# Kernel optimization log

Measured on AMD Instinct MI355X. Metric: run time of the kernel, lower is better.

Reference implementation:

```python
import jax, jax.numpy as jnp
import numpy as np

CLP_K = 9
SCL_KS = (3, 4, 3)  # scl0_k, scl1_k, scl2_k from the source


def _ste(f, x):
    # straight-through estimator: forward f(x), identity gradient
    return x + jax.lax.stop_gradient(f(x) - x)


def floor_ste(x):
    return _ste(jnp.floor, x)


def round_ste(x):
    return _ste(jnp.round, x)


def conv_t(x, w, b):
    # torch F.conv_transpose2d with kernel 5, stride 2, padding 2, output_padding 1
    # expressed as an lhs-dilated conv; w is torch layout [in, out, kh, kw]
    k = w.shape[-1]
    wc = jnp.flip(w, axis=(-2, -1)).transpose(1, 0, 2, 3)  # -> [out, in, kh, kw]
    lo = k - 1 - 2           # k-1-padding = 2
    hi = k - 1 - 2 + 1       # + output_padding = 3
    y = jax.lax.conv_general_dilated(
        x, wc, window_strides=(1, 1), padding=[(lo, hi), (lo, hi)],
        lhs_dilation=(2, 2), dimension_numbers=('NCHW', 'OIHW', 'NCHW'))
    return y + b[None, :, None, None]


def split_deconv(x, w, b, split):
    # sum of `split` transposed convs with floor((round(W)+j)/split) quantized weights
    out = 0.0
    for j in range(split):
        wj = floor_ste((round_ste(w) + j) / split)
        bj = floor_ste((round_ste(b) + j) / split)
        out = out + conv_t(x, wj, bj)
    return out


def _g_s_forward(x, ws, bs, ms, relus, dv, Bits, split):
    # clp[i] = round((2^Bits - 1) / relus[i] * 2^(16+clp_k))
    clp = jnp.round((2.0 ** Bits - 1.0) / relus * 2.0 ** (16 + CLP_K))
    for i in range(3):
        x = split_deconv(x, ws[i], bs[i], split)
        x = x * ms[i][None, :, None, None]
        x = floor_ste((x + 2.0 ** (dv[i] - 1 - CLP_K)) / 2.0 ** (dv[i] - CLP_K))
        x = jnp.clip(x, 0.0, clp[i])
        sk = SCL_KS[i]
        scl = floor_ste((relus[i] + 2.0 ** (sk - 1)) / 2.0 ** sk)
        x = floor_ste((x * scl + 2.0 ** (15 + CLP_K - sk)) / 2.0 ** (16 + CLP_K - sk))
    x = split_deconv(x, ws[3], bs[3], split)
    x = x * ms[3][None, :, None, None]
    x = floor_ste((x + 2.0 ** (dv[3] - 9)) / 2.0 ** (dv[3] - 8))
    return x / 255.0


def setup_inputs() -> dict:
    key = jax.random.key(0)
    ks = jax.random.split(key, 16)
    N, M = 192, 320
    B, h, w = 1, 48, 48
    x = jax.random.randint(ks[0], (B, M, h, w), 0, 256).astype(jnp.float32)
    w1 = jax.random.normal(ks[1], (M, N, 5, 5), jnp.float32) * 20.0
    b1 = jax.random.normal(ks[2], (N,), jnp.float32) * 20.0
    w2 = jax.random.normal(ks[3], (N, N, 5, 5), jnp.float32) * 20.0
    b2 = jax.random.normal(ks[4], (N,), jnp.float32) * 20.0
    w3 = jax.random.normal(ks[5], (N, N, 5, 5), jnp.float32) * 20.0
    b3 = jax.random.normal(ks[6], (N,), jnp.float32) * 20.0
    w4 = jax.random.normal(ks[7], (N, 3, 5, 5), jnp.float32) * 20.0
    b4 = jax.random.normal(ks[8], (3,), jnp.float32) * 20.0
    muls0 = jax.random.randint(ks[9], (N,), 1, 1000).astype(jnp.float32)
    muls1 = jax.random.randint(ks[10], (N,), 1, 1000).astype(jnp.float32)
    muls2 = jax.random.randint(ks[11], (N,), 1, 1000).astype(jnp.float32)
    muls3 = jax.random.randint(ks[12], (3,), 1, 1000).astype(jnp.float32)
    relus = jnp.array([40000.0, 36000.0, 30000.0], jnp.float32)
    muls_dvds = jnp.array([24, 24, 24, 24], jnp.int32)
    return {"x": x, "w1": w1, "b1": b1, "w2": w2, "b2": b2, "w3": w3,
            "b3": b3, "w4": w4, "b4": b4, "muls0": muls0, "muls1": muls1,
            "muls2": muls2, "muls3": muls3, "relus": relus,
            "muls_dvds": muls_dvds, "Bits": 8, "split": 4}


def reference(x, w1, b1, w2, b2, w3, b3, w4, b4,
              muls0, muls1, muls2, muls3, relus, muls_dvds, Bits, split):
    dv = muls_dvds.astype(jnp.float32)
    ws = (w1, w2, w3, w4)
    bs = (b1, b2, b3, b4)
    ms = (muls0, muls1, muls2, muls3)
    return _g_s_forward(x, ws, bs, ms, relus, dv, int(Bits), int(split))
```

## Files before the change

kernel.cpp:

```cpp
#include <hip/hip_runtime.h>
#include <cmath>


typedef int int4v  __attribute__((ext_vector_type(4)));
typedef int int16v __attribute__((ext_vector_type(16)));

#define GLOBAL_AS __attribute__((address_space(1)))
#define LDS_AS    __attribute__((address_space(3)))

__device__ __forceinline__ void dma16(const signed char* g, signed char* l) {
    __builtin_amdgcn_global_load_lds((const GLOBAL_AS int*)g, (LDS_AS int*)l,
                                     16, 0, 0);
}

__device__ __forceinline__ void tap_to_k(int t, int& ky, int& kx) {
    if (t < 9)       { int dy = t/3,  dx = t%3;                   ky = 4-2*dy; kx = 4-2*dx; }
    else if (t < 15) { int u = t-9;   int dy = u/2, dx = 1+(u&1);  ky = 4-2*dy; kx = 5-2*dx; }
    else if (t < 21) { int u = t-15;  int dy = 1+u/3, dx = u%3;    ky = 5-2*dy; kx = 4-2*dx; }
    else             { int u = t-21;  int dy = 1+u/2, dx = 1+(u&1); ky = 5-2*dy; kx = 5-2*dx; }
}

__global__ __launch_bounds__(256)
void convert_x_t(const float* __restrict__ x, signed char* __restrict__ xh,
                 int* __restrict__ tsz, int ts_count, int C, int HW) {
    if (blockIdx.x == 0 && blockIdx.y == 0)
        for (int i = threadIdx.x; i < ts_count; i += 256) tsz[i] = 0;
    __shared__ float t[64][65];
    const int p0 = blockIdx.x * 64;
    const int c0 = blockIdx.y * 64;
    const int pL = threadIdx.x & 63;
    const int r0 = threadIdx.x >> 6;
    #pragma unroll
    for (int k = 0; k < 16; ++k) {
        int ciL = r0 * 16 + k;
        t[ciL][pL] = x[(size_t)(c0 + ciL) * HW + p0 + pL];
    }
    __syncthreads();
    #pragma unroll
    for (int k = 0; k < 16; ++k) {
        int pL2 = r0 * 16 + k;
        xh[(size_t)(p0 + pL2) * C + c0 + pL] = (signed char)((int)t[pL][pL2] - 128);
    }
}

__global__ __launch_bounds__(256)
void packA(const float* __restrict__ w1, const float* __restrict__ w2,
           const float* __restrict__ w3,
           signed char* __restrict__ p1, signed char* __restrict__ p2,
           signed char* __restrict__ p3,
           int* __restrict__ t1, int* __restrict__ t2, int* __restrict__ t3) {
    const int layer = blockIdx.y;
    const float* w = (layer == 0) ? w1 : (layer == 1) ? w2 : w3;
    signed char* out = (layer == 0) ? p1 : (layer == 1) ? p2 : p3;
    int* ts = (layer == 0) ? t1 : (layer == 1) ? t2 : t3;
    const int Cout = 192;
    const int s = blockIdx.x;
    if (layer > 0 && s >= 36) return;
    const int qs = s / 6, nb = s % 6;

    __shared__ __align__(16) signed char ls[25600];
    __shared__ int lsum[4][32];
    if (threadIdx.x < 128) ((int*)lsum)[threadIdx.x] = 0;
    __syncthreads();

    #pragma unroll
    for (int k = 0; k < 4; ++k) {
        const int pidx = threadIdx.x + k * 256;
        const int cil = pidx >> 5;
        const int col = pidx & 31;
        const int ci = qs * 32 + cil;
        const int co = nb * 32 + col;
        const float* wr = w + (size_t)(ci * Cout + co) * 25;
        const int half = cil >> 4, j = cil & 15;
        const int base = (half * 32 + col) * 16 + j;
        int psum[4] = {0, 0, 0, 0};
        #pragma unroll
        for (int t = 0; t < 25; ++t) {
            int ky, kx; tap_to_k(t, ky, kx);
            float v = rintf(wr[ky * 5 + kx]);
            v = fminf(fmaxf(v, -128.0f), 127.0f);
            int iv = (int)v;
            ls[t * 1024 + base] = (signed char)iv;
            psum[((ky & 1) << 1) | (kx & 1)] += iv;
        }
        #pragma unroll
        for (int p = 0; p < 4; ++p) atomicAdd(&lsum[p][col], psum[p]);
    }
    __syncthreads();

    signed char* dst = out + (size_t)s * 25600;
    for (int i = threadIdx.x; i < 1600; i += 256)
        *(int4v*)&dst[i * 16] = *(const int4v*)&ls[i * 16];
    if (threadIdx.x < 128) {
        const int p = threadIdx.x >> 5, col = threadIdx.x & 31;
        atomicAdd(&ts[p * Cout + nb * 32 + col], lsum[p][col]);
    }
}

__global__ void pack_w4_i8(const float* __restrict__ w, signed char* __restrict__ wpk) {
    int idx = blockIdx.x * blockDim.x + threadIdx.x;
    if (idx >= 6 * 9 * 64 * 16) return;
    int j    = idx & 15;
    int lane = (idx >> 4) & 63;
    int rem  = idx >> 10;
    int s9   = rem % 9;
    int qs   = rem / 9;
    int col  = lane & 31;
    int co   = col & 7;
    int p    = col >> 3;
    int py = p >> 1, px = p & 1;
    int dy = s9 / 3, dx = s9 % 3;
    int ci = qs * 32 + ((lane >> 5) << 4) + j;
    bool part = (py == 0 || dy >= 1) && (px == 0 || dx >= 1);
    float v = 0.0f;
    if (co < 3 && part) {
        int ky = py ? 5 - 2 * dy : 4 - 2 * dy;
        int kx = px ? 5 - 2 * dx : 4 - 2 * dx;
        v = rintf(w[(size_t)(ci * 3 + co) * 25 + ky * 5 + kx]);
        v = fminf(fmaxf(v, -128.0f), 127.0f);
    }
    wpk[idx] = (signed char)(int)v;
}

__global__ __launch_bounds__(64)
void tap_w4(const float* __restrict__ w, int* __restrict__ ts) {
    const int Cin = 192, Cout = 3;
    const int i = blockIdx.x;
    const int co = i % Cout, p = i / Cout;
    const int py = p >> 1, px = p & 1;
    const int nky = (5 - py + 1) >> 1;
    const int nkx = (5 - px + 1) >> 1;
    const int ntap = nky * nkx;
    int s = 0;
    for (int idx = threadIdx.x; idx < Cin * ntap; idx += 64) {
        const int ci = idx / ntap;
        const int u  = idx - ci * ntap;
        const int ky = py + 2 * (u / nkx);
        const int kx = px + 2 * (u % nkx);
        float v = rintf(w[(size_t)(ci * Cout + co) * 25 + ky * 5 + kx]);
        v = fminf(fmaxf(v, -128.0f), 127.0f);
        s += (int)v;
    }
    #pragma unroll
    for (int off = 32; off > 0; off >>= 1)
        s += __shfl_down(s, off, 64);
    if (threadIdx.x == 0) ts[i] = s;
}

__device__ __forceinline__ constexpr int role_nt(int role, int s9) {
    constexpr int NT0[9] = {1,1,1,1,2,2,1,2,2};
    constexpr int NT1[9] = {0,1,1,1,2,2,1,2,2};
    return role == 0 ? NT0[s9] : NT1[s9];
}
__device__ __forceinline__ constexpr int role_tap(int role, int s9, int u) {
    constexpr int T0[9][2] = {{0,0},{1,0},{2,0},{3,0},{4,21},{5,22},{6,0},{7,23},{8,24}};
    constexpr int T1[9][2] = {{0,0},{9,0},{10,0},{15,0},{11,16},{12,17},{18,0},{13,19},{14,20}};
    return role == 0 ? T0[s9][u] : T1[s9][u];
}
__device__ __forceinline__ constexpr int role_acc(int role, int s9, int u) {
    constexpr int A0[9][2] = {{0,0},{0,0},{0,0},{0,0},{0,1},{0,1},{0,0},{0,1},{0,1}};
    constexpr int A1[9][2] = {{0,0},{0,0},{0,0},{1,0},{0,1},{0,1},{1,0},{0,1},{0,1}};
    return role == 0 ? A0[s9][u] : A1[s9][u];
}

template<int ROLE, int R>
__device__ __forceinline__ void compute_role(const signed char* xsb, const signed char* bsb,
                                             int16v (&acc)[R][2], const int (&p0)[R],
                                             int half, int lane) {
    #pragma unroll
    for (int s9 = 0; s9 < 9; ++s9) {
        if (role_nt(ROLE, s9) == 0) continue;
        const int dy = s9 / 3, dx = s9 % 3;
        int4v a[R];
        #pragma unroll
        for (int r = 0; r < R; ++r)
            a[r] = *(const int4v*)&xsb[(p0[r] + dy * 18 + dx) * 48 + half * 16];
        #pragma unroll
        for (int u = 0; u < 2; ++u) {
            if (u < role_nt(ROLE, s9)) {
                int4v b = *(const int4v*)&bsb[role_tap(ROLE, s9, u) * 1024 + lane * 16];
                const int ai = role_acc(ROLE, s9, u);
                #pragma unroll
                for (int r = 0; r < R; ++r)
                    acc[r][ai] = __builtin_amdgcn_mfma_i32_32x32x32_i8(a[r], b, acc[r][ai], 0, 0, 0);
            }
        }
    }
}

template<int MW, int R>
__global__ __launch_bounds__(MW * 64, MW == 8 ? 4 : 3)
void deconv_v11(const signed char* __restrict__ xin, const signed char* __restrict__ wpk,
                const float* __restrict__ bias, const float* __restrict__ muls,
                const int* __restrict__ tsum,
                const float* __restrict__ relus, const int* __restrict__ dvds,
                const int* __restrict__ bitsp,
                int layer, int Cin, int Cout, int NT, int Hq, int Wq,
                int NB, int NQX, int T8,
                signed char* __restrict__ outp) {
    constexpr int PAIRS = MW / 2;
    constexpr int NROW = PAIRS * R * 2 + 2;
    constexpr int NPIX = NROW * 18;
    constexpr int THREADS = MW * 64;
    constexpr int XC = NPIX * 2;
    constexpr int XI = (XC + THREADS - 1) / THREADS;
    constexpr int BC = 1600;
    constexpr int BTI = (BC + THREADS - 1) / THREADS;

    __shared__ __align__(16) signed char xs[NPIX * 48];
    __shared__ __align__(16) signed char bs[2][25600];

    const int tid  = threadIdx.x;
    const int lane = tid & 63;
    const int wid  = tid >> 6;
    const int pairId = wid >> 1;
    const int role   = wid & 1;

    int nb, qx, qy;
    {
        const int bi = blockIdx.x;
        if (T8 > 0) {
            const int xcd = bi & 7, j = bi >> 3;
            const int tl = j / NB, n = j - tl * NB;
            const int tile = xcd * T8 + tl;
            nb = n; qx = tile % NQX; qy = tile / NQX;
        } else {
            nb = bi % NB;
            const int s = bi / NB;
            qx = s % NQX; qy = s / NQX;
        }
    }
    const int qx0 = qx * 16;
    const int qy0 = qy * (PAIRS * R * 2);
    const int n0  = nb * 32;

    int16v acc[R][2];
    #pragma unroll
    for (int r = 0; r < R; ++r)
        #pragma unroll
        for (int p = 0; p < 2; ++p)
            #pragma unroll
            for (int e = 0; e < 16; ++e) acc[r][p][e] = 0;

    const int half   = lane >> 5;
    const int rowbit = (lane >> 4) & 1;
    const int col    = lane & 15;
    int p0[R];
    #pragma unroll
    for (int r = 0; r < R; ++r)
        p0[r] = ((pairId * R + r) * 2 + rowbit) * 18 + col;

    int4v xreg[XI];
    auto load_x = [&](int ck) {
        #pragma unroll
        for (int t = 0; t < XI; ++t) {
            int i = tid + t * THREADS;
            if (i < XC) {
                int pix = i >> 1, g = i & 1;
                int rr = pix / 18, cc = pix - rr * 18;
                int y = qy0 - 1 + rr, xx = qx0 - 1 + cc;
                int4v v = {(int)0x80808080, (int)0x80808080,
                           (int)0x80808080, (int)0x80808080};
                if ((unsigned)y < (unsigned)Hq && (unsigned)xx < (unsigned)Wq)
                    v = *(const int4v*)&xin[((size_t)y * Wq + xx) * Cin + ck + g * 16];
                xreg[t] = v;
            }
        }
    };
    auto store_x = [&]() {
        #pragma unroll
        for (int t = 0; t < XI; ++t) {
            int i = tid + t * THREADS;
            if (i < XC) {
                int pix = i >> 1, g = i & 1;
                *(int4v*)&xs[pix * 48 + g * 16] = xreg[t];
            }
        }
    };
    auto dma_b = [&](const signed char* wslab, signed char* dst) {
        #pragma unroll
        for (int t = 0; t < BTI; ++t) {
            int i = tid + t * THREADS;
            if (i < BC)
                dma16(wslab + (size_t)i * 16, dst + (size_t)i * 16);
        }
    };

    load_x(0);
    dma_b(wpk + (size_t)nb * 25600, bs[0]);
    for (int ck = 0; ck < Cin; ck += 32) {
        const int cbuf = (ck >> 5) & 1;
        __syncthreads();
        store_x();
        __syncthreads();
        if (ck + 32 < Cin) {
            load_x(ck + 32);
            dma_b(wpk + (size_t)(((ck >> 5) + 1) * NT + nb) * 25600, bs[cbuf ^ 1]);
        }
        if (role == 0) compute_role<0, R>(xs, bs[cbuf], acc, p0, half, lane);
        else           compute_role<1, R>(xs, bs[cbuf], acc, p0, half, lane);
    }

    const int dv = dvds[layer];
    float add1 = ldexpf(1.0f, dv - 10);
    float inv1 = ldexpf(1.0f, -(dv - 9));
    const float relu = relus[layer];
    const int sk = (layer == 1) ? 4 : 3;
    const float bitsv = ldexpf(1.0f, bitsp[0]) - 1.0f;
    float clp, scl;
    {
        #pragma clang fp contract(off)
        clp = rintf(bitsv / relu * 33554432.0f);
        scl = floorf((relu + ldexpf(1.0f, sk - 1)) * ldexpf(1.0f, -sk));
    }
    float add2 = ldexpf(1.0f, 24 - sk);
    float inv2 = ldexpf(1.0f, -(25 - sk));

    const int co = n0 + (lane & 31);
    float bq = rintf(bias[co]);
    float mm = muls[co];
    int pmap[2];
    pmap[0] = role == 0 ? 0 : 1;
    pmap[1] = role == 0 ? 3 : 2;
    int fullp[2];
    #pragma unroll
    for (int a = 0; a < 2; ++a) fullp[a] = tsum[pmap[a] * Cout + co];

    const int Wout = Wq * 2;

    #pragma unroll
    for (int r = 0; r < R; ++r) {
        #pragma unroll
        for (int a = 0; a < 2; ++a) {
            const int p = pmap[a];
            const int py = p >> 1, px = p & 1;
            #pragma unroll
            for (int reg = 0; reg < 16; ++reg) {
                const int mrow = (reg & 3) + 8 * (reg >> 2) + 4 * (lane >> 5);
                const int qy2 = qy0 + (pairId * R + r) * 2 + (mrow >> 4);
                const int qx2 = qx0 + (mrow & 15);
                float v = (float)(acc[r][a][reg] + 128 * fullp[a]);
                {
                    #pragma clang fp contract(off)
                    v = (v + bq) * mm;
                    v = floorf((v + add1) * inv1);
                    v = fminf(fmaxf(v, 0.0f), clp);
                    v = floorf((v * scl + add2) * inv2);
                }
                const int oy = 2 * qy2 + py, ox = 2 * qx2 + px;
                outp[((size_t)oy * Wout + ox) * Cout + co] = (signed char)((int)v - 128);
            }
        }
    }
}

__global__ __launch_bounds__(512, 4)
void deconv_final_v11(const signed char* __restrict__ xin, const signed char* __restrict__ wpk,
                      const float* __restrict__ bias, const float* __restrict__ muls,
                      const int* __restrict__ tsum, const int* __restrict__ dvds,
                      int Cin, int Hq, int Wq, float* __restrict__ outp) {
    constexpr int R = 2, MW = 8;
    constexpr int NROW = MW * R * 2 + 2;
    constexpr int NPIX = NROW * 18;
    constexpr int THREADS = 512;
    constexpr int XC = NPIX * 2;
    constexpr int XI = (XC + THREADS - 1) / THREADS;
    constexpr int BC = 576;
    constexpr int BTI = (BC + THREADS - 1) / THREADS;

    __shared__ __align__(16) signed char xs[NPIX * 48];
    __shared__ __align__(16) signed char bs[2][9216];

    const int tid  = threadIdx.x;
    const int lane = tid & 63;
    const int wid  = tid >> 6;
    const int qx0  = blockIdx.y * 16;
    const int qy0  = blockIdx.z * (MW * R * 2);

    int16v acc[R];
    #pragma unroll
    for (int r = 0; r < R; ++r)
        #pragma unroll
        for (int e = 0; e < 16; ++e) acc[r][e] = 0;

    const int half   = lane >> 5;
    const int rowbit = (lane >> 4) & 1;
    const int col    = lane & 15;
    int p0[R];
    #pragma unroll
    for (int r = 0; r < R; ++r)
        p0[r] = ((wid * R + r) * 2 + rowbit) * 18 + col;

    int4v xreg[XI];
    auto load_x = [&](int ck) {
        #pragma unroll
        for (int t = 0; t < XI; ++t) {
            int i = tid + t * THREADS;
            if (i < XC) {
                int pix = i >> 1, g = i & 1;
                int rr = pix / 18, cc = pix - rr * 18;
                int y = qy0 - 1 + rr, xx = qx0 - 1 + cc;
                int4v v = {(int)0x80808080, (int)0x80808080,
                           (int)0x80808080, (int)0x80808080};
                if ((unsigned)y < (unsigned)Hq && (unsigned)xx < (unsigned)Wq)
                    v = *(const int4v*)&xin[((size_t)y * Wq + xx) * Cin + ck + g * 16];
                xreg[t] = v;
            }
        }
    };
    auto store_x = [&]() {
        #pragma unroll
        for (int t = 0; t < XI; ++t) {
            int i = tid + t * THREADS;
            if (i < XC) {
                int pix = i >> 1, g = i & 1;
                *(int4v*)&xs[pix * 48 + g * 16] = xreg[t];
            }
        }
    };
    auto dma_b = [&](const signed char* wslab, signed char* dst) {
        #pragma unroll
        for (int t = 0; t < BTI; ++t) {
            int i = tid + t * THREADS;
            if (i < BC)
                dma16(wslab + (size_t)i * 16, dst + (size_t)i * 16);
        }
    };

    load_x(0);
    dma_b(wpk, bs[0]);
    for (int ck = 0; ck < Cin; ck += 32) {
        const int cbuf = (ck >> 5) & 1;
        __syncthreads();
        store_x();
        __syncthreads();
        if (ck + 32 < Cin) {
            load_x(ck + 32);
            dma_b(wpk + (size_t)((ck >> 5) + 1) * 9216, bs[cbuf ^ 1]);
        }

        #pragma unroll
        for (int s9 = 0; s9 < 9; ++s9) {
            const int dy = s9 / 3, dx = s9 % 3;
            int4v b = *(const int4v*)&bs[cbuf][s9 * 1024 + lane * 16];
            #pragma unroll
            for (int r = 0; r < R; ++r) {
                int4v a = *(const int4v*)&xs[(p0[r] + dy * 18 + dx) * 48 + half * 16];
                acc[r] = __builtin_amdgcn_mfma_i32_32x32x32_i8(a, b, acc[r], 0, 0, 0);
            }
        }
    }

    const int dv = dvds[3];
    const float add1 = ldexpf(1.0f, dv - 9);
    const float inv1 = ldexpf(1.0f, -(dv - 8));

    const int coln = lane & 31;
    const int co = coln & 7;
    const int p  = coln >> 3;
    const int py = p >> 1, px = p & 1;
    const bool valid = (co < 3);
    float bq = 0.f, mm = 0.f;
    int fp = 0;
    if (valid) { bq = rintf(bias[co]); mm = muls[co]; fp = tsum[p * 3 + co]; }

    const int Wout = Wq * 2, Hout = Hq * 2;
    #pragma unroll
    for (int r = 0; r < R; ++r) {
        #pragma unroll
        for (int reg = 0; reg < 16; ++reg) {
            const int mrow = (reg & 3) + 8 * (reg >> 2) + 4 * (lane >> 5);
            const int qy = qy0 + (wid * R + r) * 2 + (mrow >> 4);
            const int qx = qx0 + (mrow & 15);
            float v = (float)(acc[r][reg] + 128 * fp);
            {
                #pragma clang fp contract(off)
                v = (v + bq) * mm;
                v = floorf((v + add1) * inv1);
                v = v / 255.0f;
            }
            if (valid) {
                const int oy = 2 * qy + py, ox = 2 * qx + px;
                outp[((size_t)co * Hout + oy) * Wout + ox] = v;
            }
        }
    }
}

extern "C" void kernel_launch(void* const* d_in, const int* in_sizes, int n_in,
                              void* d_out, int out_size, void* d_ws, size_t ws_size,
                              hipStream_t stream) {
    const float* x  = (const float*)d_in[0];
    const float* w1 = (const float*)d_in[1];
    const float* b1 = (const float*)d_in[2];
    const float* w2 = (const float*)d_in[3];
    const float* b2 = (const float*)d_in[4];
    const float* w3 = (const float*)d_in[5];
    const float* b3 = (const float*)d_in[6];
    const float* w4 = (const float*)d_in[7];
    const float* b4 = (const float*)d_in[8];
    const float* m0 = (const float*)d_in[9];
    const float* m1 = (const float*)d_in[10];
    const float* m2 = (const float*)d_in[11];
    const float* m3 = (const float*)d_in[12];
    const float* relus = (const float*)d_in[13];
    const int* dvds = (const int*)d_in[14];
    const int* bitsp = (const int*)d_in[15];

    signed char* wsb = (signed char*)d_ws;
    size_t o = 0;
    signed char* wpk1 = wsb + o; o += (size_t)10 * 6 * 25600;
    signed char* wpk2 = wsb + o; o += (size_t)6 * 6 * 25600;
    signed char* wpk3 = wsb + o; o += (size_t)6 * 6 * 25600;
    signed char* wpk4 = wsb + o; o += (size_t)6 * 9216;
    int* ts1 = (int*)(wsb + o); o += 4 * 192 * 4;
    int* ts2 = (int*)(wsb + o); o += 4 * 192 * 4;
    int* ts3 = (int*)(wsb + o); o += 4 * 192 * 4;
    int* ts4 = (int*)(wsb + o); o += 4 * 4 * 4;
    o = (o + 15) & ~(size_t)15;
    signed char* xh = wsb + o; o += (size_t)48 * 48 * 320;
    signed char* a1 = wsb + o; o += (size_t)96 * 96 * 192;
    signed char* a2 = wsb + o; o += (size_t)192 * 192 * 192;
    signed char* a3 = wsb + o; o += (size_t)384 * 384 * 192;

    const int ts_count = 4 * 192 * 3 + 4 * 4;

    convert_x_t<<<dim3(36, 5), 256, 0, stream>>>(x, xh, ts1, ts_count, 320, 48 * 48);
    packA<<<dim3(60, 3), 256, 0, stream>>>(w1, w2, w3, wpk1, wpk2, wpk3, ts1, ts2, ts3);
    pack_w4_i8<<<(6 * 9 * 1024 + 255) / 256, 256, 0, stream>>>(w4, wpk4);
    tap_w4<<<12, 64, 0, stream>>>(w4, ts4);

    deconv_v11<4, 2><<<108, 256, 0, stream>>>(
        xh, wpk1, b1, m0, ts1, relus, dvds, bitsp, 0, 320, 192, 6, 48, 48,
        6, 3, 0, a1);
    deconv_v11<8, 2><<<216, 512, 0, stream>>>(
        a1, wpk2, b2, m1, ts2, relus, dvds, bitsp, 1, 192, 192, 6, 96, 96,
        6, 6, 0, a2);
    deconv_v11<8, 2><<<864, 512, 0, stream>>>(
        a2, wpk3, b3, m2, ts3, relus, dvds, bitsp, 2, 192, 192, 6, 192, 192,
        6, 12, 18, a3);
    deconv_final_v11<<<dim3(1, 24, 12), 512, 0, stream>>>(
        a3, wpk4, b4, m3, ts4, dvds, 192, 384, 384, (float*)d_out);
}
```

Measured before the change: 212.9 us.

## Double-buffer activations via direct global-to-LDS DMA and retune block shapes

The activation tile is now loaded with direct global-to-LDS DMA into a double buffer, using precomputed source pointers and a shared padding buffer for out-of-bounds pixels. This replaces the register-staged load and store and removes one barrier per channel chunk. The LDS activation stride drops from 48 to 32 bytes. The change also merges the w4 pack and tap-sum kernels into the weight prep kernel, shrinks the layer-2 and final blocks to 4 waves with more blocks, and sets all launch bounds to 4 blocks per SM. The 32-byte stride may increase LDS bank conflicts, and the doubled activation buffer raises LDS use.

```diff
diff --git a/kernel.cpp b/kernel.cpp
--- a/kernel.cpp
+++ b/kernel.cpp
@@ -22,9 +22,12 @@
 
 __global__ __launch_bounds__(256)
 void convert_x_t(const float* __restrict__ x, signed char* __restrict__ xh,
-                 int* __restrict__ tsz, int ts_count, int C, int HW) {
-    if (blockIdx.x == 0 && blockIdx.y == 0)
+                 int* __restrict__ tsz, int ts_count, int C, int HW,
+                 signed char* __restrict__ xpad) {
+    if (blockIdx.x == 0 && blockIdx.y == 0) {
         for (int i = threadIdx.x; i < ts_count; i += 256) tsz[i] = 0;
+        if (threadIdx.x < 128) ((int*)xpad)[threadIdx.x] = (int)0x80808080;
+    }
     __shared__ float t[64][65];
     const int p0 = blockIdx.x * 64;
     const int c0 = blockIdx.y * 64;
@@ -44,12 +47,66 @@
 }
 
 __global__ __launch_bounds__(256)
-void packA(const float* __restrict__ w1, const float* __restrict__ w2,
-           const float* __restrict__ w3,
-           signed char* __restrict__ p1, signed char* __restrict__ p2,
-           signed char* __restrict__ p3,
-           int* __restrict__ t1, int* __restrict__ t2, int* __restrict__ t3) {
+void prep_pack(const float* __restrict__ w1, const float* __restrict__ w2,
+               const float* __restrict__ w3, const float* __restrict__ w4,
+               signed char* __restrict__ p1, signed char* __restrict__ p2,
+               signed char* __restrict__ p3, signed char* __restrict__ p4,
+               int* __restrict__ t1, int* __restrict__ t2, int* __restrict__ t3,
+               int* __restrict__ t4) {
     const int layer = blockIdx.y;
+    if (layer == 3) {
+        const int bx = blockIdx.x;
+        if (bx < 54) {
+            #pragma unroll
+            for (int k = 0; k < 4; ++k) {
+                int idx = bx * 1024 + k * 256 + threadIdx.x;
+                int j    = idx & 15;
+                int lane = (idx >> 4) & 63;
+                int rem  = idx >> 10;
+                int s9   = rem % 9;
+                int qs   = rem / 9;
+                int col  = lane & 31;
+                int co   = col & 7;
+                int p    = col >> 3;
+                int py = p >> 1, px = p & 1;
+                int dy = s9 / 3, dx = s9 % 3;
+                int ci = qs * 32 + ((lane >> 5) << 4) + j;
+                bool part = (py == 0 || dy >= 1) && (px == 0 || dx >= 1);
+                float v = 0.0f;
+                if (co < 3 && part) {
+                    int ky = py ? 5 - 2 * dy : 4 - 2 * dy;
+                    int kx = px ? 5 - 2 * dx : 4 - 2 * dx;
+                    v = rintf(w4[(size_t)(ci * 3 + co) * 25 + ky * 5 + kx]);
+                    v = fminf(fmaxf(v, -128.0f), 127.0f);
+                }
+                p4[idx] = (signed char)(int)v;
+            }
+        } else if (threadIdx.x < 128) {
+            const int Cin = 192, Cout = 3;
+            const int u = (bx - 54) * 2 + (threadIdx.x >> 6);
+            const int lane = threadIdx.x & 63;
+            const int co = u % Cout, p = u / Cout;
+            const int py = p >> 1, px = p & 1;
+            const int nky = (5 - py + 1) >> 1;
+            const int nkx = (5 - px + 1) >> 1;
+            const int ntap = nky * nkx;
+            int s = 0;
+            for (int idx = lane; idx < Cin * ntap; idx += 64) {
+                const int ci = idx / ntap;
+                const int uu = idx - ci * ntap;
+                const int ky = py + 2 * (uu / nkx);
+                const int kx = px + 2 * (uu % nkx);
+                float v = rintf(w4[(size_t)(ci * Cout + co) * 25 + ky * 5 + kx]);
+                v = fminf(fmaxf(v, -128.0f), 127.0f);
+                s += (int)v;
+            }
+            #pragma unroll
+            for (int off = 32; off > 0; off >>= 1)
+                s += __shfl_down(s, off, 64);
+            if (lane == 0) t4[u] = s;
+        }
+        return;
+    }
     const float* w = (layer == 0) ? w1 : (layer == 1) ? w2 : w3;
     signed char* out = (layer == 0) ? p1 : (layer == 1) ? p2 : p3;
     int* ts = (layer == 0) ? t1 : (layer == 1) ? t2 : t3;
@@ -97,56 +154,6 @@
     }
 }
 
-__global__ void pack_w4_i8(const float* __restrict__ w, signed char* __restrict__ wpk) {
-    int idx = blockIdx.x * blockDim.x + threadIdx.x;
-    if (idx >= 6 * 9 * 64 * 16) return;
-    int j    = idx & 15;
-    int lane = (idx >> 4) & 63;
-    int rem  = idx >> 10;
-    int s9   = rem % 9;
-    int qs   = rem / 9;
-    int col  = lane & 31;
-    int co   = col & 7;
-    int p    = col >> 3;
-    int py = p >> 1, px = p & 1;
-    int dy = s9 / 3, dx = s9 % 3;
-    int ci = qs * 32 + ((lane >> 5) << 4) + j;
-    bool part = (py == 0 || dy >= 1) && (px == 0 || dx >= 1);
-    float v = 0.0f;
-    if (co < 3 && part) {
-        int ky = py ? 5 - 2 * dy : 4 - 2 * dy;
-        int kx = px ? 5 - 2 * dx : 4 - 2 * dx;
-        v = rintf(w[(size_t)(ci * 3 + co) * 25 + ky * 5 + kx]);
-        v = fminf(fmaxf(v, -128.0f), 127.0f);
-    }
-    wpk[idx] = (signed char)(int)v;
-}
-
-__global__ __launch_bounds__(64)
-void tap_w4(const float* __restrict__ w, int* __restrict__ ts) {
-    const int Cin = 192, Cout = 3;
-    const int i = blockIdx.x;
-    const int co = i % Cout, p = i / Cout;
-    const int py = p >> 1, px = p & 1;
-    const int nky = (5 - py + 1) >> 1;
-    const int nkx = (5 - px + 1) >> 1;
-    const int ntap = nky * nkx;
-    int s = 0;
-    for (int idx = threadIdx.x; idx < Cin * ntap; idx += 64) {
-        const int ci = idx / ntap;
-        const int u  = idx - ci * ntap;
-        const int ky = py + 2 * (u / nkx);
-        const int kx = px + 2 * (u % nkx);
-        float v = rintf(w[(size_t)(ci * Cout + co) * 25 + ky * 5 + kx]);
-        v = fminf(fmaxf(v, -128.0f), 127.0f);
-        s += (int)v;
-    }
-    #pragma unroll
-    for (int off = 32; off > 0; off >>= 1)
-        s += __shfl_down(s, off, 64);
-    if (threadIdx.x == 0) ts[i] = s;
-}
-
 __device__ __forceinline__ constexpr int role_nt(int role, int s9) {
     constexpr int NT0[9] = {1,1,1,1,2,2,1,2,2};
     constexpr int NT1[9] = {0,1,1,1,2,2,1,2,2};
@@ -174,7 +181,7 @@
         int4v a[R];
         #pragma unroll
         for (int r = 0; r < R; ++r)
-            a[r] = *(const int4v*)&xsb[(p0[r] + dy * 18 + dx) * 48 + half * 16];
+            a[r] = *(const int4v*)&xsb[(p0[r] + dy * 18 + dx) * 32 + half * 16];
         #pragma unroll
         for (int u = 0; u < 2; ++u) {
             if (u < role_nt(ROLE, s9)) {
@@ -189,25 +196,26 @@
 }
 
 template<int MW, int R>
-__global__ __launch_bounds__(MW * 64, MW == 8 ? 4 : 3)
-void deconv_v11(const signed char* __restrict__ xin, const signed char* __restrict__ wpk,
+__global__ __launch_bounds__(MW * 64, 4)
+void deconv_v12(const signed char* __restrict__ xin, const signed char* __restrict__ wpk,
                 const float* __restrict__ bias, const float* __restrict__ muls,
                 const int* __restrict__ tsum,
                 const float* __restrict__ relus, const int* __restrict__ dvds,
-                const int* __restrict__ bitsp,
+                const int* __restrict__ bitsp, const signed char* __restrict__ xpad,
                 int layer, int Cin, int Cout, int NT, int Hq, int Wq,
                 int NB, int NQX, int T8,
                 signed char* __restrict__ outp) {
     constexpr int PAIRS = MW / 2;
-    constexpr int NROW = PAIRS * R * 2 + 2;
+    constexpr int QROWS = PAIRS * R * 2;
+    constexpr int NROW = QROWS + 2;
     constexpr int NPIX = NROW * 18;
     constexpr int THREADS = MW * 64;
     constexpr int XC = NPIX * 2;
     constexpr int XI = (XC + THREADS - 1) / THREADS;
     constexpr int BC = 1600;
-    constexpr int BTI = (BC + THREADS - 1) / THREADS;
-
-    __shared__ __align__(16) signed char xs[NPIX * 48];
+    constexpr int BI = (BC + THREADS - 1) / THREADS;
+
+    __shared__ __align__(16) signed char xs[2][NPIX * 32];
     __shared__ __align__(16) signed char bs[2][25600];
 
     const int tid  = threadIdx.x;
@@ -231,7 +239,7 @@
         }
     }
     const int qx0 = qx * 16;
-    const int qy0 = qy * (PAIRS * R * 2);
+    const int qy0 = qy * QROWS;
     const int n0  = nb * 32;
 
     int16v acc[R][2];
@@ -250,55 +258,48 @@
     for (int r = 0; r < R; ++r)
         p0[r] = ((pairId * R + r) * 2 + rowbit) * 18 + col;
 
-    int4v xreg[XI];
-    auto load_x = [&](int ck) {
+    const signed char* xsrc[XI];
+    #pragma unroll
+    for (int t = 0; t < XI; ++t) {
+        int i = tid + t * THREADS;
+        xsrc[t] = xpad;
+        if (i < XC) {
+            int pix = i >> 1, g = i & 1;
+            int rr = pix / 18, cc = pix - rr * 18;
+            int y = qy0 - 1 + rr, xx = qx0 - 1 + cc;
+            bool ok = (unsigned)y < (unsigned)Hq && (unsigned)xx < (unsigned)Wq;
+            xsrc[t] = ok ? (xin + ((size_t)y * Wq + xx) * Cin + g * 16)
+                         : (xpad + g * 16);
+        }
+    }
+
+    auto dma_x = [&](int ck, int b) {
         #pragma unroll
         for (int t = 0; t < XI; ++t) {
             int i = tid + t * THREADS;
-            if (i < XC) {
-                int pix = i >> 1, g = i & 1;
-                int rr = pix / 18, cc = pix - rr * 18;
-                int y = qy0 - 1 + rr, xx = qx0 - 1 + cc;
-                int4v v = {(int)0x80808080, (int)0x80808080,
-                           (int)0x80808080, (int)0x80808080};
-                if ((unsigned)y < (unsigned)Hq && (unsigned)xx < (unsigned)Wq)
-                    v = *(const int4v*)&xin[((size_t)y * Wq + xx) * Cin + ck + g * 16];
-                xreg[t] = v;
-            }
+            if (i < XC) dma16(xsrc[t] + ck, &xs[b][i * 16]);
         }
     };
-    auto store_x = [&]() {
-        #pragma unroll
-        for (int t = 0; t < XI; ++t) {
+    auto dma_b = [&](int cs, int b) {
+        const signed char* ws = wpk + (size_t)(cs * NT + nb) * 25600;
+        #pragma unroll
+        for (int t = 0; t < BI; ++t) {
             int i = tid + t * THREADS;
-            if (i < XC) {
-                int pix = i >> 1, g = i & 1;
-                *(int4v*)&xs[pix * 48 + g * 16] = xreg[t];
-            }
+            if (i < BC) dma16(ws + (size_t)i * 16, &bs[b][i * 16]);
         }
     };
-    auto dma_b = [&](const signed char* wslab, signed char* dst) {
-        #pragma unroll
-        for (int t = 0; t < BTI; ++t) {
-            int i = tid + t * THREADS;
-            if (i < BC)
-                dma16(wslab + (size_t)i * 16, dst + (size_t)i * 16);
-        }
-    };
-
-    load_x(0);
-    dma_b(wpk + (size_t)nb * 25600, bs[0]);
+
+    dma_x(0, 0);
+    dma_b(0, 0);
     for (int ck = 0; ck < Cin; ck += 32) {
-        const int cbuf = (ck >> 5) & 1;
-        __syncthreads();
-        store_x();
+        const int cb = (ck >> 5) & 1;
         __syncthreads();
         if (ck + 32 < Cin) {
-            load_x(ck + 32);
-            dma_b(wpk + (size_t)(((ck >> 5) + 1) * NT + nb) * 25600, bs[cbuf ^ 1]);
-        }
-        if (role == 0) compute_role<0, R>(xs, bs[cbuf], acc, p0, half, lane);
-        else           compute_role<1, R>(xs, bs[cbuf], acc, p0, half, lane);
+            dma_x(ck + 32, cb ^ 1);
+            dma_b((ck >> 5) + 1, cb ^ 1);
+        }
+        if (role == 0) compute_role<0, R>(xs[cb], bs[cb], acc, p0, half, lane);
+        else           compute_role<1, R>(xs[cb], bs[cb], acc, p0, half, lane);
     }
 
     const int dv = dvds[layer];
@@ -354,28 +355,30 @@
     }
 }
 
-__global__ __launch_bounds__(512, 4)
-void deconv_final_v11(const signed char* __restrict__ xin, const signed char* __restrict__ wpk,
+__global__ __launch_bounds__(256, 4)
+void deconv_final_v12(const signed char* __restrict__ xin, const signed char* __restrict__ wpk,
                       const float* __restrict__ bias, const float* __restrict__ muls,
                       const int* __restrict__ tsum, const int* __restrict__ dvds,
+                      const signed char* __restrict__ xpad,
                       int Cin, int Hq, int Wq, float* __restrict__ outp) {
-    constexpr int R = 2, MW = 8;
-    constexpr int NROW = MW * R * 2 + 2;
+    constexpr int R = 2, MW = 4;
+    constexpr int QROWS = MW * R * 2;
+    constexpr int NROW = QROWS + 2;
     constexpr int NPIX = NROW * 18;
-    constexpr int THREADS = 512;
+    constexpr int THREADS = 256;
     constexpr int XC = NPIX * 2;
     constexpr int XI = (XC + THREADS - 1) / THREADS;
     constexpr int BC = 576;
-    constexpr int BTI = (BC + THREADS - 1) / THREADS;
-
-    __shared__ __align__(16) signed char xs[NPIX * 48];
+    constexpr int BI = (BC + THREADS - 1) / THREADS;
+
+    __shared__ __align__(16) signed char xs[2][NPIX * 32];
     __shared__ __align__(16) signed char bs[2][9216];
 
     const int tid  = threadIdx.x;
     const int lane = tid & 63;
     const int wid  = tid >> 6;
     const int qx0  = blockIdx.y * 16;
-    const int qy0  = blockIdx.z * (MW * R * 2);
+    const int qy0  = blockIdx.z * QROWS;
 
     int16v acc[R];
     #pragma unroll
@@ -391,61 +394,53 @@
     for (int r = 0; r < R; ++r)
         p0[r] = ((wid * R + r) * 2 + rowbit) * 18 + col;
 
-    int4v xreg[XI];
-    auto load_x = [&](int ck) {
+    const signed char* xsrc[XI];
+    #pragma unroll
+    for (int t = 0; t < XI; ++t) {
+        int i = tid + t * THREADS;
+        xsrc[t] = xpad;
+        if (i < XC) {
+            int pix = i >> 1, g = i & 1;
+            int rr = pix / 18, cc = pix - rr * 18;
+            int y = qy0 - 1 + rr, xx = qx0 - 1 + cc;
+            bool ok = (unsigned)y < (unsigned)Hq && (unsigned)xx < (unsigned)Wq;
+            xsrc[t] = ok ? (xin + ((size_t)y * Wq + xx) * Cin + g * 16)
+                         : (xpad + g * 16);
+        }
+    }
+
+    auto dma_x = [&](int ck, int b) {
         #pragma unroll
         for (int t = 0; t < XI; ++t) {
             int i = tid + t * THREADS;
-            if (i < XC) {
-                int pix = i >> 1, g = i & 1;
-                int rr = pix / 18, cc = pix - rr * 18;
-                int y = qy0 - 1 + rr, xx = qx0 - 1 + cc;
-                int4v v = {(int)0x80808080, (int)0x80808080,
-                           (int)0x80808080, (int)0x80808080};
-                if ((unsigned)y < (unsigned)Hq && (unsigned)xx < (unsigned)Wq)
-                    v = *(const int4v*)&xin[((size_t)y * Wq + xx) * Cin + ck + g * 16];
-                xreg[t] = v;
-            }
+            if (i < XC) dma16(xsrc[t] + ck, &xs[b][i * 16]);
         }
     };
-    auto store_x = [&]() {
-        #pragma unroll
-        for (int t = 0; t < XI; ++t) {
+    auto dma_b = [&](int cs, int b) {
+        const signed char* ws = wpk + (size_t)cs * 9216;
+        #pragma unroll
+        for (int t = 0; t < BI; ++t) {
             int i = tid + t * THREADS;
-            if (i < XC) {
-                int pix = i >> 1, g = i & 1;
-                *(int4v*)&xs[pix * 48 + g * 16] = xreg[t];
-            }
+            if (i < BC) dma16(ws + (size_t)i * 16, &bs[b][i * 16]);
         }
     };
-    auto dma_b = [&](const signed char* wslab, signed char* dst) {
-        #pragma unroll
-        for (int t = 0; t < BTI; ++t) {
-            int i = tid + t * THREADS;
-            if (i < BC)
-                dma16(wslab + (size_t)i * 16, dst + (size_t)i * 16);
-        }
-    };
-
-    load_x(0);
-    dma_b(wpk, bs[0]);
+
+    dma_x(0, 0);
+    dma_b(0, 0);
     for (int ck = 0; ck < Cin; ck += 32) {
-        const int cbuf = (ck >> 5) & 1;
-        __syncthreads();
-        store_x();
+        const int cb = (ck >> 5) & 1;
         __syncthreads();
         if (ck + 32 < Cin) {
-            load_x(ck + 32);
-            dma_b(wpk + (size_t)((ck >> 5) + 1) * 9216, bs[cbuf ^ 1]);
-        }
-
+            dma_x(ck + 32, cb ^ 1);
+            dma_b((ck >> 5) + 1, cb ^ 1);
+        }
         #pragma unroll
         for (int s9 = 0; s9 < 9; ++s9) {
             const int dy = s9 / 3, dx = s9 % 3;
-            int4v b = *(const int4v*)&bs[cbuf][s9 * 1024 + lane * 16];
+            int4v b = *(const int4v*)&bs[cb][s9 * 1024 + lane * 16];
             #pragma unroll
             for (int r = 0; r < R; ++r) {
-                int4v a = *(const int4v*)&xs[(p0[r] + dy * 18 + dx) * 48 + half * 16];
+                int4v a = *(const int4v*)&xs[cb][(p0[r] + dy * 18 + dx) * 32 + half * 16];
                 acc[r] = __builtin_amdgcn_mfma_i32_32x32x32_i8(a, b, acc[r], 0, 0, 0);
             }
         }
@@ -518,6 +513,7 @@
     int* ts3 = (int*)(wsb + o); o += 4 * 192 * 4;
     int* ts4 = (int*)(wsb + o); o += 4 * 4 * 4;
     o = (o + 15) & ~(size_t)15;
+    signed char* xpad = wsb + o; o += 512;
     signed char* xh = wsb + o; o += (size_t)48 * 48 * 320;
     signed char* a1 = wsb + o; o += (size_t)96 * 96 * 192;
     signed char* a2 = wsb + o; o += (size_t)192 * 192 * 192;
@@ -525,20 +521,20 @@
 
     const int ts_count = 4 * 192 * 3 + 4 * 4;
 
-    convert_x_t<<<dim3(36, 5), 256, 0, stream>>>(x, xh, ts1, ts_count, 320, 48 * 48);
-    packA<<<dim3(60, 3), 256, 0, stream>>>(w1, w2, w3, wpk1, wpk2, wpk3, ts1, ts2, ts3);
-    pack_w4_i8<<<(6 * 9 * 1024 + 255) / 256, 256, 0, stream>>>(w4, wpk4);
-    tap_w4<<<12, 64, 0, stream>>>(w4, ts4);
-
-    deconv_v11<4, 2><<<108, 256, 0, stream>>>(
-        xh, wpk1, b1, m0, ts1, relus, dvds, bitsp, 0, 320, 192, 6, 48, 48,
+    convert_x_t<<<dim3(36, 5), 256, 0, stream>>>(x, xh, ts1, ts_count, 320, 48 * 48, xpad);
+    prep_pack<<<dim3(60, 4), 256, 0, stream>>>(w1, w2, w3, w4,
+                                               wpk1, wpk2, wpk3, wpk4,
+                                               ts1, ts2, ts3, ts4);
+
+    deconv_v12<4, 2><<<108, 256, 0, stream>>>(
+        xh, wpk1, b1, m0, ts1, relus, dvds, bitsp, xpad, 0, 320, 192, 6, 48, 48,
         6, 3, 0, a1);
-    deconv_v11<8, 2><<<216, 512, 0, stream>>>(
-        a1, wpk2, b2, m1, ts2, relus, dvds, bitsp, 1, 192, 192, 6, 96, 96,
+    deconv_v12<4, 2><<<432, 256, 0, stream>>>(
+        a1, wpk2, b2, m1, ts2, relus, dvds, bitsp, xpad, 1, 192, 192, 6, 96, 96,
         6, 6, 0, a2);
-    deconv_v11<8, 2><<<864, 512, 0, stream>>>(
-        a2, wpk3, b3, m2, ts3, relus, dvds, bitsp, 2, 192, 192, 6, 192, 192,
+    deconv_v12<8, 2><<<864, 512, 0, stream>>>(
+        a2, wpk3, b3, m2, ts3, relus, dvds, bitsp, xpad, 2, 192, 192, 6, 192, 192,
         6, 12, 18, a3);
-    deconv_final_v11<<<dim3(1, 24, 12), 512, 0, stream>>>(
-        a3, wpk4, b4, m3, ts4, dvds, 192, 384, 384, (float*)d_out);
-}
+    deconv_final_v12<<<dim3(1, 24, 24), 256, 0, stream>>>(
+        a3, wpk4, b4, m3, ts4, dvds, xpad, 192, 384, 384, (float*)d_out);
+}
```

Result: faster. 200.7 us (-5.7%).
